# Kernel optimization log

Measured on AMD Instinct MI355X. Metric: run time of the kernel, lower is better.

Reference implementation:

```python
import jax, jax.numpy as jnp
import numpy as np

N_NODES = 50000


def _gcn_norm(edge_index, num_nodes):
    """PyG GCNConv normalization: add self-loops, symmetric deg^{-1/2} weights."""
    loops = jnp.arange(num_nodes, dtype=edge_index.dtype)
    src = jnp.concatenate([edge_index[0], loops])
    dst = jnp.concatenate([edge_index[1], loops])
    deg = jax.ops.segment_sum(jnp.ones_like(dst, dtype=jnp.float32), dst,
                              num_segments=num_nodes)
    dinv = jax.lax.rsqrt(jnp.maximum(deg, 1.0))  # self-loops guarantee deg>=1
    norm = dinv[src] * dinv[dst]                 # [E + N]
    return src, dst, norm


def _gcn_conv(x, W, b, src, dst, norm, num_nodes):
    h = x @ W                                    # [N, out] dense GEMM
    msg = h[src] * norm[:, None]                 # gather + scale
    agg = jax.ops.segment_sum(msg, dst, num_segments=num_nodes)
    return agg + b


def setup_inputs() -> dict:
    key = jax.random.key(0)
    ks = jax.random.split(key, 8)
    d = 128
    scale = 1.0 / np.sqrt(d)
    emb = jax.random.normal(ks[0], (N_NODES, d), dtype=jnp.float32)
    W1 = jax.random.normal(ks[1], (d, d), dtype=jnp.float32) * scale
    W2 = jax.random.normal(ks[2], (d, d), dtype=jnp.float32) * scale
    W3 = jax.random.normal(ks[3], (d, d), dtype=jnp.float32) * scale
    b1 = jnp.zeros((d,), dtype=jnp.float32)
    b2 = jnp.zeros((d,), dtype=jnp.float32)
    b3 = jnp.zeros((d,), dtype=jnp.float32)
    edge_index = jax.random.randint(ks[4], (2, 600000), 0, N_NODES, dtype=jnp.int64)
    return {"emb": emb, "W1": W1, "b1": b1, "W2": W2, "b2": b2,
            "W3": W3, "b3": b3, "edge_index": edge_index}


def reference(emb, W1, b1, W2, b2, W3, b3, edge_index):
    # Eval-mode forward: F.dropout(training=False) is identity.
    src, dst, norm = _gcn_norm(edge_index, N_NODES)
    x = emb
    x = jax.nn.relu(_gcn_conv(x, W1, b1, src, dst, norm, N_NODES))
    x = jax.nn.relu(_gcn_conv(x, W2, b2, src, dst, norm, N_NODES))
    x = _gcn_conv(x, W3, b3, src, dst, norm, N_NODES)
    x = x.at[0].set(0.0)  # x[0] = zeros(x.shape[1])
    return x
```

## Files before the change

kernel.cpp:

```cpp
#include <hip/hip_runtime.h>
#include <hip/hip_fp16.h>

#define NN 50000
#define D 128
#define STRIDE 64

typedef __attribute__((ext_vector_type(16))) float f32x16;
typedef _Float16 h16;
typedef __attribute__((ext_vector_type(2))) _Float16 h16x2;
typedef __attribute__((ext_vector_type(8))) _Float16 h16x8;

struct alignas(16) H8 { h16 h[8]; };


__global__ __launch_bounds__(256) void fill_kernel(const int* __restrict__ srcA,
                                                   const int* __restrict__ dstA,
                                                   int* __restrict__ cnt,
                                                   int* __restrict__ slots, int nquad) {
    int t = blockIdx.x * 256 + threadIdx.x;
    if (t >= nquad) return;
    int4 s4 = ((const int4*)srcA)[t];
    int4 d4 = ((const int4*)dstA)[t];
    int p0 = atomicAdd(&cnt[d4.x], 1);
    int p1 = atomicAdd(&cnt[d4.y], 1);
    int p2 = atomicAdd(&cnt[d4.z], 1);
    int p3 = atomicAdd(&cnt[d4.w], 1);
    if (p0 < STRIDE - 4) slots[d4.x * STRIDE + p0] = s4.x;
    if (p1 < STRIDE - 4) slots[d4.y * STRIDE + p1] = s4.y;
    if (p2 < STRIDE - 4) slots[d4.z * STRIDE + p2] = s4.z;
    if (p3 < STRIDE - 4) slots[d4.w * STRIDE + p3] = s4.w;
}

__global__ __launch_bounds__(256) void dinv_kernel(const int* __restrict__ cnt,
                                                   float* __restrict__ dinv) {
    int i = blockIdx.x * 256 + threadIdx.x;
    if (i < NN) dinv[i] = rsqrtf((float)cnt[i] + 1.0f);
}

__global__ __launch_bounds__(256) void weight_kernel(const int* __restrict__ cnt,
                                                     const float* __restrict__ dinv,
                                                     const int* __restrict__ slots,
                                                     int2* __restrict__ csr2) {
    int idx = blockIdx.x * 256 + threadIdx.x;
    int node = idx >> 6;
    int j = idx & 63;
    if (node >= NN) return;
    int c = cnt[node];
    int pc = min((c + 4) & ~3, STRIDE);
    if (j < pc) {
        int2 v;
        if (j < c) {
            int s = slots[idx];
            v = make_int2(s, __float_as_int(dinv[s]));
        } else if (j == c) {
            v = make_int2(node, __float_as_int(dinv[node]));
        } else {
            v = make_int2(0, 0);
        }
        csr2[idx] = v;
    }
}

__global__ __launch_bounds__(256, 2) void gemm_mfma(const void* __restrict__ Xv, int x_is_f32,
                                                    const float* __restrict__ W,
                                                    h16* __restrict__ H, int M,
                                                    int* __restrict__ cnt_zero) {
    __shared__ h16 Ws[32768];
    {
        const int l  = threadIdx.x & 63;
        const int ct = threadIdx.x >> 6;
        const int n  = ct * 32 + (l & 31);
        const int lh = l >> 5;
#pragma unroll
        for (int ks = 0; ks < 8; ks++) {
            const int kbase = ks * 16 + lh * 8;
            H8 hi8, lo8;
#pragma unroll
            for (int j = 0; j < 8; j++) {
                float w = W[(kbase + j) * D + n];
                h16 hi = (h16)w;
                hi8.h[j] = hi;
                lo8.h[j] = (h16)(w - (float)hi);
            }
            const int base = ((ks * 4 + ct) * 64 + l) * 8;
            *(H8*)(Ws + base)         = hi8;
            *(H8*)(Ws + base + 16384) = lo8;
        }
        if (cnt_zero && blockIdx.x < 196) {
            int i = blockIdx.x * 256 + threadIdx.x;
            if (i < NN) cnt_zero[i] = 0;
        }
    }
    __syncthreads();

    const int wave = threadIdx.x >> 6;
    const int lane = threadIdx.x & 63;
    const int row0 = blockIdx.x * 128 + wave * 32;
    const int arow = min(row0 + (lane & 31), M - 1);
    const int koff = (lane >> 5) * 8;

    f32x16 acc[4] = {};

#pragma unroll
    for (int ks = 0; ks < 8; ks++) {
        h16x8 ahi, alo;
        if (x_is_f32) {
            const float* p = (const float*)Xv + (size_t)arow * D + koff + ks * 16;
            float4 fa = *(const float4*)p;
            float4 fb = *(const float4*)(p + 4);
            float f[8] = {fa.x, fa.y, fa.z, fa.w, fb.x, fb.y, fb.z, fb.w};
#pragma unroll
            for (int j = 0; j < 8; j++) {
                h16 hi = (h16)f[j];
                ahi[j] = hi;
                alo[j] = (h16)(f[j] - (float)hi);
            }
        } else {
            const h16* p = (const h16*)Xv + (size_t)arow * D + koff + ks * 16;
            ahi = *(const h16x8*)p;
        }
#pragma unroll
        for (int ct = 0; ct < 4; ct++) {
            const int base = ((ks * 4 + ct) * 64 + lane) * 8;
            h16x8 bhi = *(const h16x8*)(Ws + base);
            h16x8 blo = *(const h16x8*)(Ws + base + 16384);
            acc[ct] = __builtin_amdgcn_mfma_f32_32x32x16_f16(ahi, bhi, acc[ct], 0, 0, 0);
            acc[ct] = __builtin_amdgcn_mfma_f32_32x32x16_f16(ahi, blo, acc[ct], 0, 0, 0);
            if (x_is_f32)
                acc[ct] = __builtin_amdgcn_mfma_f32_32x32x16_f16(alo, bhi, acc[ct], 0, 0, 0);
        }
    }

    const int col0 = lane & 31;
    const int rbase = row0 + 4 * (lane >> 5);
#pragma unroll
    for (int ct = 0; ct < 4; ct++) {
#pragma unroll
        for (int r = 0; r < 16; r++) {
            int row = rbase + (r & 3) + 8 * (r >> 2);
            if (row < M) H[(size_t)row * D + ct * 32 + col0] = (h16)acc[ct][r];
        }
    }
}

__global__ __launch_bounds__(256) void agg_kernel(const h16* __restrict__ H,
                                                  const float* __restrict__ dinv,
                                                  const int* __restrict__ cnt,
                                                  const int2* __restrict__ csr2,
                                                  const float* __restrict__ bias,
                                                  h16* __restrict__ out16,
                                                  float* __restrict__ out32,
                                                  int n, int mode) {
    int node = blockIdx.x * 4 + (threadIdx.x >> 6);
    if (node >= n) return;
    int lane = threadIdx.x & 63;
    int col = lane * 2;

    float ax = 0.f, ay = 0.f, bx = 0.f, by = 0.f;

    int c = __builtin_amdgcn_readfirstlane(cnt[node]);
    int s = node * STRIDE;
    int e = s + min((c + 4) & ~3, STRIDE);

    for (int p = s; p < e; p += 4) {
        int2 w0 = csr2[p];
        int2 w1 = csr2[p + 1];
        int2 w2 = csr2[p + 2];
        int2 w3 = csr2[p + 3];
        h16x2 v0 = *(const h16x2*)(H + (size_t)w0.x * D + col);
        h16x2 v1 = *(const h16x2*)(H + (size_t)w1.x * D + col);
        h16x2 v2 = *(const h16x2*)(H + (size_t)w2.x * D + col);
        h16x2 v3 = *(const h16x2*)(H + (size_t)w3.x * D + col);
        float f0 = __int_as_float(w0.y), f1 = __int_as_float(w1.y);
        float f2 = __int_as_float(w2.y), f3 = __int_as_float(w3.y);
        ax = fmaf(f0, (float)v0[0], ax); ay = fmaf(f0, (float)v0[1], ay);
        bx = fmaf(f1, (float)v1[0], bx); by = fmaf(f1, (float)v1[1], by);
        ax = fmaf(f2, (float)v2[0], ax); ay = fmaf(f2, (float)v2[1], ay);
        bx = fmaf(f3, (float)v3[0], bx); by = fmaf(f3, (float)v3[1], by);
    }
    ax += bx; ay += by;

    float di = dinv[node];
    float2 bb = *(const float2*)(bias + col);
    float rx = fmaf(di, ax, bb.x);
    float ry = fmaf(di, ay, bb.y);
    if (mode == 0) {
        rx = fmaxf(rx, 0.f); ry = fmaxf(ry, 0.f);
        h16x2 o; o[0] = (h16)rx; o[1] = (h16)ry;
        *(h16x2*)(out16 + (size_t)node * D + col) = o;
    } else {
        if (node == 0) { rx = 0.f; ry = 0.f; }
        *(float2*)(out32 + (size_t)node * D + col) = make_float2(rx, ry);
    }
}


extern "C" void kernel_launch(void* const* d_in, const int* in_sizes, int n_in,
                              void* d_out, int out_size, void* d_ws, size_t ws_size,
                              hipStream_t stream) {
    const float* emb = (const float*)d_in[0];
    const float* W1  = (const float*)d_in[1];
    const float* b1  = (const float*)d_in[2];
    const float* W2  = (const float*)d_in[3];
    const float* b2  = (const float*)d_in[4];
    const float* W3  = (const float*)d_in[5];
    const float* b3  = (const float*)d_in[6];
    const int*   ei  = (const int*)d_in[7];

    const int E = in_sizes[7] / 2;
    const int* srcA = ei;
    const int* dstA = ei + E;
    float* out = (float*)d_out;

    char* ws = (char*)d_ws;
    size_t off = 0;
    auto alloc = [&](size_t bytes) -> void* {
        void* p = ws + off;
        off = (off + bytes + 255) & ~(size_t)255;
        return p;
    };
    h16* h      = (h16*)alloc((size_t)NN * D * 2);
    h16* x16    = (h16*)alloc((size_t)NN * D * 2);
    float* dinv = (float*)alloc((size_t)NN * 4);
    int* cnt    = (int*)alloc((size_t)NN * 4);
    int* slots  = (int*)alloc((size_t)NN * STRIDE * 4);
    int2* csr2  = (int2*)alloc((size_t)NN * STRIDE * 8);

    const int T = 256;
    const int gemm_grid = (NN + 127) / 128;
    const int agg_grid  = (NN + 3) / 4;
    const int nquad = E / 4;

    gemm_mfma<<<gemm_grid, T, 0, stream>>>(emb, 1, W1, h, NN, cnt);
    fill_kernel<<<(nquad + T - 1) / T, T, 0, stream>>>(srcA, dstA, cnt, slots, nquad);
    dinv_kernel<<<(NN + T - 1) / T, T, 0, stream>>>(cnt, dinv);
    weight_kernel<<<(NN * STRIDE + T - 1) / T, T, 0, stream>>>(cnt, dinv, slots, csr2);
    agg_kernel<<<agg_grid, T, 0, stream>>>(h, dinv, cnt, csr2, b1, x16, nullptr, NN, 0);
    gemm_mfma<<<gemm_grid, T, 0, stream>>>(x16, 0, W2, h, NN, nullptr);
    agg_kernel<<<agg_grid, T, 0, stream>>>(h, dinv, cnt, csr2, b2, x16, nullptr, NN, 0);
    gemm_mfma<<<gemm_grid, T, 0, stream>>>(x16, 0, W3, h, NN, nullptr);
    agg_kernel<<<agg_grid, T, 0, stream>>>(h, dinv, cnt, csr2, b3, nullptr, out, NN, 1);
}
```

Baseline: 263.5 us.

## Split each node's neighbors across wave halves with 8-byte gathers, drop dinv kernel

```diff
diff --git a/kernel.cpp b/kernel.cpp
--- a/kernel.cpp
+++ b/kernel.cpp
@@ -7,7 +7,7 @@
 
 typedef __attribute__((ext_vector_type(16))) float f32x16;
 typedef _Float16 h16;
-typedef __attribute__((ext_vector_type(2))) _Float16 h16x2;
+typedef __attribute__((ext_vector_type(4))) _Float16 h16x4;
 typedef __attribute__((ext_vector_type(8))) _Float16 h16x8;
 
 struct alignas(16) H8 { h16 h[8]; };
@@ -16,29 +16,32 @@
 __global__ __launch_bounds__(256) void fill_kernel(const int* __restrict__ srcA,
                                                    const int* __restrict__ dstA,
                                                    int* __restrict__ cnt,
-                                                   int* __restrict__ slots, int nquad) {
+                                                   int* __restrict__ slots, int noct) {
     int t = blockIdx.x * 256 + threadIdx.x;
-    if (t >= nquad) return;
-    int4 s4 = ((const int4*)srcA)[t];
-    int4 d4 = ((const int4*)dstA)[t];
-    int p0 = atomicAdd(&cnt[d4.x], 1);
-    int p1 = atomicAdd(&cnt[d4.y], 1);
-    int p2 = atomicAdd(&cnt[d4.z], 1);
-    int p3 = atomicAdd(&cnt[d4.w], 1);
-    if (p0 < STRIDE - 4) slots[d4.x * STRIDE + p0] = s4.x;
-    if (p1 < STRIDE - 4) slots[d4.y * STRIDE + p1] = s4.y;
-    if (p2 < STRIDE - 4) slots[d4.z * STRIDE + p2] = s4.z;
-    if (p3 < STRIDE - 4) slots[d4.w * STRIDE + p3] = s4.w;
-}
-
-__global__ __launch_bounds__(256) void dinv_kernel(const int* __restrict__ cnt,
-                                                   float* __restrict__ dinv) {
-    int i = blockIdx.x * 256 + threadIdx.x;
-    if (i < NN) dinv[i] = rsqrtf((float)cnt[i] + 1.0f);
+    if (t >= noct) return;
+    int4 sa = ((const int4*)srcA)[2 * t];
+    int4 sb = ((const int4*)srcA)[2 * t + 1];
+    int4 da = ((const int4*)dstA)[2 * t];
+    int4 db = ((const int4*)dstA)[2 * t + 1];
+    int p0 = atomicAdd(&cnt[da.x], 1);
+    int p1 = atomicAdd(&cnt[da.y], 1);
+    int p2 = atomicAdd(&cnt[da.z], 1);
+    int p3 = atomicAdd(&cnt[da.w], 1);
+    int p4 = atomicAdd(&cnt[db.x], 1);
+    int p5 = atomicAdd(&cnt[db.y], 1);
+    int p6 = atomicAdd(&cnt[db.z], 1);
+    int p7 = atomicAdd(&cnt[db.w], 1);
+    if (p0 < STRIDE - 8) slots[da.x * STRIDE + p0] = sa.x;
+    if (p1 < STRIDE - 8) slots[da.y * STRIDE + p1] = sa.y;
+    if (p2 < STRIDE - 8) slots[da.z * STRIDE + p2] = sa.z;
+    if (p3 < STRIDE - 8) slots[da.w * STRIDE + p3] = sa.w;
+    if (p4 < STRIDE - 8) slots[db.x * STRIDE + p4] = sb.x;
+    if (p5 < STRIDE - 8) slots[db.y * STRIDE + p5] = sb.y;
+    if (p6 < STRIDE - 8) slots[db.z * STRIDE + p6] = sb.z;
+    if (p7 < STRIDE - 8) slots[db.w * STRIDE + p7] = sb.w;
 }
 
 __global__ __launch_bounds__(256) void weight_kernel(const int* __restrict__ cnt,
-                                                     const float* __restrict__ dinv,
                                                      const int* __restrict__ slots,
                                                      int2* __restrict__ csr2) {
     int idx = blockIdx.x * 256 + threadIdx.x;
@@ -46,14 +49,14 @@
     int j = idx & 63;
     if (node >= NN) return;
     int c = cnt[node];
-    int pc = min((c + 4) & ~3, STRIDE);
+    int pc = min((c + 8) & ~7, STRIDE);
     if (j < pc) {
         int2 v;
         if (j < c) {
             int s = slots[idx];
-            v = make_int2(s, __float_as_int(dinv[s]));
+            v = make_int2(s, __float_as_int(rsqrtf((float)cnt[s] + 1.0f)));
         } else if (j == c) {
-            v = make_int2(node, __float_as_int(dinv[node]));
+            v = make_int2(node, __float_as_int(rsqrtf((float)c + 1.0f)));
         } else {
             v = make_int2(0, 0);
         }
@@ -144,7 +147,6 @@
 }
 
 __global__ __launch_bounds__(256) void agg_kernel(const h16* __restrict__ H,
-                                                  const float* __restrict__ dinv,
                                                   const int* __restrict__ cnt,
                                                   const int2* __restrict__ csr2,
                                                   const float* __restrict__ bias,
@@ -154,43 +156,53 @@
     int node = blockIdx.x * 4 + (threadIdx.x >> 6);
     if (node >= n) return;
     int lane = threadIdx.x & 63;
-    int col = lane * 2;
-
-    float ax = 0.f, ay = 0.f, bx = 0.f, by = 0.f;
-
-    int c = __builtin_amdgcn_readfirstlane(cnt[node]);
-    int s = node * STRIDE;
-    int e = s + min((c + 4) & ~3, STRIDE);
-
-    for (int p = s; p < e; p += 4) {
-        int2 w0 = csr2[p];
-        int2 w1 = csr2[p + 1];
-        int2 w2 = csr2[p + 2];
-        int2 w3 = csr2[p + 3];
-        h16x2 v0 = *(const h16x2*)(H + (size_t)w0.x * D + col);
-        h16x2 v1 = *(const h16x2*)(H + (size_t)w1.x * D + col);
-        h16x2 v2 = *(const h16x2*)(H + (size_t)w2.x * D + col);
-        h16x2 v3 = *(const h16x2*)(H + (size_t)w3.x * D + col);
-        float f0 = __int_as_float(w0.y), f1 = __int_as_float(w1.y);
-        float f2 = __int_as_float(w2.y), f3 = __int_as_float(w3.y);
-        ax = fmaf(f0, (float)v0[0], ax); ay = fmaf(f0, (float)v0[1], ay);
-        bx = fmaf(f1, (float)v1[0], bx); by = fmaf(f1, (float)v1[1], by);
-        ax = fmaf(f2, (float)v2[0], ax); ay = fmaf(f2, (float)v2[1], ay);
-        bx = fmaf(f3, (float)v3[0], bx); by = fmaf(f3, (float)v3[1], by);
-    }
-    ax += bx; ay += by;
-
-    float di = dinv[node];
-    float2 bb = *(const float2*)(bias + col);
-    float rx = fmaf(di, ax, bb.x);
-    float ry = fmaf(di, ay, bb.y);
-    if (mode == 0) {
-        rx = fmaxf(rx, 0.f); ry = fmaxf(ry, 0.f);
-        h16x2 o; o[0] = (h16)rx; o[1] = (h16)ry;
-        *(h16x2*)(out16 + (size_t)node * D + col) = o;
-    } else {
-        if (node == 0) { rx = 0.f; ry = 0.f; }
-        *(float2*)(out32 + (size_t)node * D + col) = make_float2(rx, ry);
+    int half = lane >> 5;
+    int col = (lane & 31) * 4;
+
+    int unode = __builtin_amdgcn_readfirstlane(node);
+    int c = __builtin_amdgcn_readfirstlane(cnt[unode]);
+    int s = unode * STRIDE;
+    int e = s + min((c + 8) & ~7, STRIDE);
+
+    float a0 = 0.f, a1 = 0.f, a2 = 0.f, a3 = 0.f;
+
+    for (int p = s; p < e; p += 8) {
+        int2 wq[8];
+#pragma unroll
+        for (int j = 0; j < 8; j++) wq[j] = csr2[p + j];
+#pragma unroll
+        for (int k = 0; k < 4; k++) {
+            int2 w = half ? wq[2 * k + 1] : wq[2 * k];
+            h16x4 v = *(const h16x4*)(H + (size_t)w.x * D + col);
+            float f = __int_as_float(w.y);
+            a0 = fmaf(f, (float)v[0], a0);
+            a1 = fmaf(f, (float)v[1], a1);
+            a2 = fmaf(f, (float)v[2], a2);
+            a3 = fmaf(f, (float)v[3], a3);
+        }
+    }
+
+    a0 += __shfl_xor(a0, 32, 64);
+    a1 += __shfl_xor(a1, 32, 64);
+    a2 += __shfl_xor(a2, 32, 64);
+    a3 += __shfl_xor(a3, 32, 64);
+
+    if (half == 0) {
+        float di = rsqrtf((float)c + 1.0f);
+        float4 bb = *(const float4*)(bias + col);
+        float r0 = fmaf(di, a0, bb.x);
+        float r1 = fmaf(di, a1, bb.y);
+        float r2 = fmaf(di, a2, bb.z);
+        float r3 = fmaf(di, a3, bb.w);
+        if (mode == 0) {
+            r0 = fmaxf(r0, 0.f); r1 = fmaxf(r1, 0.f);
+            r2 = fmaxf(r2, 0.f); r3 = fmaxf(r3, 0.f);
+            h16x4 o; o[0] = (h16)r0; o[1] = (h16)r1; o[2] = (h16)r2; o[3] = (h16)r3;
+            *(h16x4*)(out16 + (size_t)node * D + col) = o;
+        } else {
+            if (node == 0) { r0 = r1 = r2 = r3 = 0.f; }
+            *(float4*)(out32 + (size_t)node * D + col) = make_float4(r0, r1, r2, r3);
+        }
     }
 }
 
@@ -221,7 +233,6 @@
     };
     h16* h      = (h16*)alloc((size_t)NN * D * 2);
     h16* x16    = (h16*)alloc((size_t)NN * D * 2);
-    float* dinv = (float*)alloc((size_t)NN * 4);
     int* cnt    = (int*)alloc((size_t)NN * 4);
     int* slots  = (int*)alloc((size_t)NN * STRIDE * 4);
     int2* csr2  = (int2*)alloc((size_t)NN * STRIDE * 8);
@@ -229,15 +240,14 @@
     const int T = 256;
     const int gemm_grid = (NN + 127) / 128;
     const int agg_grid  = (NN + 3) / 4;
-    const int nquad = E / 4;
+    const int noct = E / 8;
 
     gemm_mfma<<<gemm_grid, T, 0, stream>>>(emb, 1, W1, h, NN, cnt);
-    fill_kernel<<<(nquad + T - 1) / T, T, 0, stream>>>(srcA, dstA, cnt, slots, nquad);
-    dinv_kernel<<<(NN + T - 1) / T, T, 0, stream>>>(cnt, dinv);
-    weight_kernel<<<(NN * STRIDE + T - 1) / T, T, 0, stream>>>(cnt, dinv, slots, csr2);
-    agg_kernel<<<agg_grid, T, 0, stream>>>(h, dinv, cnt, csr2, b1, x16, nullptr, NN, 0);
+    fill_kernel<<<(noct + T - 1) / T, T, 0, stream>>>(srcA, dstA, cnt, slots, noct);
+    weight_kernel<<<(NN * STRIDE + T - 1) / T, T, 0, stream>>>(cnt, slots, csr2);
+    agg_kernel<<<agg_grid, T, 0, stream>>>(h, cnt, csr2, b1, x16, nullptr, NN, 0);
     gemm_mfma<<<gemm_grid, T, 0, stream>>>(x16, 0, W2, h, NN, nullptr);
-    agg_kernel<<<agg_grid, T, 0, stream>>>(h, dinv, cnt, csr2, b2, x16, nullptr, NN, 0);
+    agg_kernel<<<agg_grid, T, 0, stream>>>(h, cnt, csr2, b2, x16, nullptr, NN, 0);
     gemm_mfma<<<gemm_grid, T, 0, stream>>>(x16, 0, W3, h, NN, nullptr);
-    agg_kernel<<<agg_grid, T, 0, stream>>>(h, dinv, cnt, csr2, b3, nullptr, out, NN, 1);
-}
+    agg_kernel<<<agg_grid, T, 0, stream>>>(h, cnt, csr2, b3, nullptr, out, NN, 1);
+}
```

Measured after the change: 452.5 us. 1.72x slower.
